# Performance work log

Measured on AMD Instinct MI355X. Metric: run time of the kernel, lower is better.

The kernel has to match this reference:

```python
import jax, jax.numpy as jnp
import numpy as np

B, N, H = 32, 2048, 128


def _lstm_step(c, h, x, Wi, Wh, b):
    # flax LSTMCell: gates i,f,g,o; sigmoid/sigmoid/tanh/sigmoid
    gates = x @ Wi + h @ Wh + b  # (B,N,4H)
    i, f, g, o = jnp.split(gates, 4, axis=-1)
    c_new = jax.nn.sigmoid(f) * c + jax.nn.sigmoid(i) * jnp.tanh(g)
    h_new = jax.nn.sigmoid(o) * jnp.tanh(c_new)
    return c_new, h_new


def setup_inputs() -> dict:
    key = jax.random.key(0)
    ks = jax.random.split(key, 24)
    f32 = jnp.float32
    inp = {}
    inp['node_embeddings'] = jax.random.normal(ks[0], (B, N, H), f32)
    for nm, k in zip(['hs_c0', 'hs_h0', 'hs_c1', 'hs_h1'], ks[1:5]):
        inp[nm] = jax.random.normal(k, (B, N, H), f32)
    ip = jax.random.uniform(ks[5], (B, N), f32)
    inp['instruction_pointer'] = ip / jnp.sum(ip, axis=-1, keepdims=True)
    inp['Wi0'] = jax.random.normal(ks[6], (H, 4 * H), f32) * 0.05
    inp['Wh0'] = jax.random.normal(ks[7], (H, 4 * H), f32) * 0.05
    inp['b0'] = jnp.zeros((4 * H,), f32)
    inp['Wi1'] = jax.random.normal(ks[8], (H, 4 * H), f32) * 0.05
    inp['Wh1'] = jax.random.normal(ks[9], (H, 4 * H), f32) * 0.05
    inp['b1'] = jnp.zeros((4 * H,), f32)
    inp['W_raise'] = jax.random.normal(ks[10], (4 * H, 2), f32) * 0.05
    inp['b_raise'] = jnp.zeros((2,), f32)
    inp['W_branch'] = jax.random.normal(ks[11], (4 * H, 2), f32) * 0.05
    inp['b_branch'] = jnp.zeros((2,), f32)
    inp['true_indexes'] = jax.random.randint(ks[12], (B, N), 0, N, jnp.int32)
    inp['false_indexes'] = jax.random.randint(ks[13], (B, N), 0, N, jnp.int32)
    inp['raise_indexes'] = jax.random.randint(ks[14], (B, N), 0, N, jnp.int32)
    inp['exit_node_indexes'] = jax.random.randint(ks[15], (B,), 0, N, jnp.int32)
    inp['raise_node_indexes'] = jax.random.randint(ks[16], (B,), 0, N, jnp.int32)
    inp['step_limits'] = jax.random.randint(ks[17], (B,), 0, 100, jnp.int32)
    inp['current_step'] = 5
    return inp


def reference(node_embeddings, hs_c0, hs_h0, hs_c1, hs_h1, instruction_pointer,
              Wi0, Wh0, b0, Wi1, Wh1, b1, W_raise, b_raise, W_branch, b_branch,
              true_indexes, false_indexes, raise_indexes,
              exit_node_indexes, raise_node_indexes, step_limits, current_step):
    bidx = jnp.arange(B)
    old = [hs_c0, hs_h0, hs_c1, hs_h1]

    # execute: per-node 2-layer stacked LSTM (vectorized over B,N)
    c0n, h0n = _lstm_step(hs_c0, hs_h0, node_embeddings, Wi0, Wh0, b0)
    c1n, h1n = _lstm_step(hs_c1, hs_h1, h0n, Wi1, Wh1, b1)
    contrib = [c0n, h0n, c1n, h1n]

    # mask_h: keep old state at exit node and (raise_in_ipagnn) at raise node
    def mask_nodes(hc, ho, idx):
        return hc.at[bidx, idx].set(ho[bidx, idx])
    contrib = [mask_nodes(mask_nodes(hc, ho, exit_node_indexes), ho, raise_node_indexes)
               for hc, ho in zip(contrib, old)]

    hs_emb = jnp.concatenate(contrib, axis=-1)  # (B,N,4H)

    raise_dec = jax.nn.softmax(hs_emb @ W_raise + b_raise, axis=-1)
    zero_one = jnp.array([0.0, 1.0], dtype=raise_dec.dtype)
    raise_dec = raise_dec.at[bidx, exit_node_indexes].set(zero_one)
    raise_dec = raise_dec.at[bidx, raise_node_indexes].set(zero_one)
    branch_dec = jax.nn.softmax(hs_emb @ W_branch + b_branch, axis=-1)

    p_raise = raise_dec[..., 0]
    p_noraise = raise_dec[..., 1]
    p_true = p_noraise * branch_dec[..., 0]
    p_false = p_noraise * branch_dec[..., 1]

    seg = jax.vmap(lambda v, idx: jax.ops.segment_sum(v, idx, num_segments=N))
    ip = instruction_pointer
    ip_new = (seg(p_raise * ip, raise_indexes)
              + seg(p_true * ip, true_indexes)
              + seg(p_false * ip, false_indexes))  # (B,N)
    denom = (ip_new + 1e-7)[..., None]

    wr = (p_raise * ip)[..., None]
    wt = (p_true * ip)[..., None]
    wf = (p_false * ip)[..., None]

    def agg(h):
        return (seg(h * wr, raise_indexes) + seg(h * wt, true_indexes)
                + seg(h * wf, false_indexes)) / denom
    hs_new = [agg(h) for h in contrib]

    # keep_old_if_done
    not_done = (current_step < step_limits)  # (B,)
    hs_out = [jnp.where(not_done[:, None, None], hn, ho) for hn, ho in zip(hs_new, old)]
    ip_out = jnp.where(not_done[:, None], ip_new, ip)

    # pack carry: (c0,h0,c1,h1, instruction_pointer) -> (B,N,4H+1)
    return jnp.concatenate(hs_out + [ip_out[..., None]], axis=-1)
```

## Files before the change

### kernel.cpp

```cpp
#include <hip/hip_runtime.h>
#include <stdint.h>

#define BB 32
#define NN 2048
#define HH 128
#define BN (BB*NN)

typedef short v8s __attribute__((ext_vector_type(8)));
typedef float v4f __attribute__((ext_vector_type(4)));

__device__ __forceinline__ unsigned short f2b(float f){
  union { float f; unsigned int i; } v; v.f = f;
  unsigned int x = v.i;
  unsigned int r = x + 0x7FFFu + ((x >> 16) & 1u);
  return (unsigned short)(r >> 16);
}
__device__ __forceinline__ unsigned int pk2(float a, float b){
  return (unsigned int)f2b(a) | ((unsigned int)f2b(b) << 16);
}
__device__ __forceinline__ float b2f(unsigned int s){
  union { unsigned int i; float f; } v; v.i = s << 16; return v.f;
}
__device__ __forceinline__ float frcp(float x){ return __builtin_amdgcn_rcpf(x); }
__device__ __forceinline__ float fsigm(float x){ return frcp(1.0f + __expf(-x)); }
__device__ __forceinline__ float ftanh(float x){ return 1.0f - 2.0f*frcp(1.0f + __expf(2.0f*x)); }

__global__ __launch_bounds__(512) void kswz(
    const float* __restrict__ Wi0, const float* __restrict__ Wh0,
    const float* __restrict__ Wi1, const float* __restrict__ Wh1,
    unsigned short* __restrict__ Bsw0, unsigned short* __restrict__ Bsw1){
  int idx = blockIdx.x*512 + threadIdx.x;
  int bid = idx >> 6;
  int lane = idx & 63;
  int layer = bid >> 8;
  int kc = (bid >> 5) & 7;
  int ct = bid & 31;
  const float* Wi = layer ? Wi1 : Wi0;
  const float* Wh = layer ? Wh1 : Wh0;
  unsigned short* dst = layer ? Bsw1 : Bsw0;
  int col = ct*16 + (lane & 15);
  int kbase = kc*32 + (lane >> 4)*8;
  size_t o = ((size_t)(kc*32 + ct)*64 + (size_t)lane)*8;
  #pragma unroll
  for (int j = 0; j < 8; j++){
    int k = kbase + j;
    dst[o + j] = f2b((k < 128) ? Wi[k*512 + col] : Wh[(k-128)*512 + col]);
  }
}

#define ROWSB 32
#define PA 264
#define PH 136

struct LstmLds {
  unsigned short A[ROWSB*PA];
  unsigned short H[ROWSB*PH];
  unsigned short G[ROWSB*PH];
};
struct CsrLds {
  int cnt[NN];
  int off[NN];
  int cur[NN];
  int wpart[8];
};

__global__ __launch_bounds__(512, 4) void klstm2(
    const float* __restrict__ ne,
    float* __restrict__ c0, float* __restrict__ h0,
    float* __restrict__ c1, float* __restrict__ h1,
    unsigned short* __restrict__ sc0, unsigned short* __restrict__ sh0,
    unsigned short* __restrict__ sc1, unsigned short* __restrict__ sh1,
    const unsigned short* __restrict__ Bsw0, const float* __restrict__ b0,
    const unsigned short* __restrict__ Bsw1, const float* __restrict__ b1,
    const int* __restrict__ exit_idx, const int* __restrict__ raise_idx,
    const int* __restrict__ ri, const int* __restrict__ ti,
    const int* __restrict__ fi,
    int* __restrict__ counts, int* __restrict__ offsets,
    unsigned short* __restrict__ edges,
    const int* __restrict__ step_limits, const int* __restrict__ cur_step,
    int useb)
{
  __shared__ union { LstmLds l; CsrLds c; } u;

  int tid = threadIdx.x;

  if (blockIdx.x < 32){
    int b = blockIdx.x;
    const int* rp = ri + b*NN;
    const int* tp = ti + b*NN;
    const int* fp = fi + b*NN;

    #pragma unroll
    for (int p = 0; p < 4; p++){ u.c.cnt[p*512 + tid] = 0; u.c.cur[p*512 + tid] = 0; }
    __syncthreads();

    int rv[4], tv[4], fv[4];
    #pragma unroll
    for (int p = 0; p < 4; p++){
      int n = p*512 + tid;
      rv[p] = rp[n]; tv[p] = tp[n]; fv[p] = fp[n];
      atomicAdd(&u.c.cnt[rv[p]], 1);
      atomicAdd(&u.c.cnt[tv[p]], 1);
      atomicAdd(&u.c.cnt[fv[p]], 1);
    }
    __syncthreads();

    int cc0 = u.c.cnt[4*tid], cc1 = u.c.cnt[4*tid+1];
    int cc2 = u.c.cnt[4*tid+2], cc3 = u.c.cnt[4*tid+3];
    int s = cc0 + cc1 + cc2 + cc3;
    int lane = tid & 63, wv = tid >> 6;
    int inc = s;
    #pragma unroll
    for (int d = 1; d < 64; d <<= 1){
      int t = __shfl_up(inc, d, 64);
      if (lane >= d) inc += t;
    }
    if (lane == 63) u.c.wpart[wv] = inc;
    __syncthreads();
    if (tid == 0){
      int run = 0;
      #pragma unroll
      for (int w = 0; w < 8; w++){ int t = u.c.wpart[w]; u.c.wpart[w] = run; run += t; }
    }
    __syncthreads();
    int excl = u.c.wpart[wv] + inc - s;
    u.c.off[4*tid]   = excl;
    u.c.off[4*tid+1] = excl + cc0;
    u.c.off[4*tid+2] = excl + cc0 + cc1;
    u.c.off[4*tid+3] = excl + cc0 + cc1 + cc2;
    offsets[b*NN + 4*tid]   = excl;
    offsets[b*NN + 4*tid+1] = excl + cc0;
    offsets[b*NN + 4*tid+2] = excl + cc0 + cc1;
    offsets[b*NN + 4*tid+3] = excl + cc0 + cc1 + cc2;
    counts[b*NN + 4*tid]   = cc0;
    counts[b*NN + 4*tid+1] = cc1;
    counts[b*NN + 4*tid+2] = cc2;
    counts[b*NN + 4*tid+3] = cc3;
    __syncthreads();

    size_t ebase = (size_t)b*3*NN;
    #pragma unroll
    for (int p = 0; p < 4; p++){
      int n = p*512 + tid;
      int t0 = rv[p]; int p0 = atomicAdd(&u.c.cur[t0], 1);
      edges[ebase + u.c.off[t0] + p0] = (unsigned short)n;
      int t1 = tv[p]; int p1 = atomicAdd(&u.c.cur[t1], 1);
      edges[ebase + u.c.off[t1] + p1] = (unsigned short)(n | (1<<11));
      int t2 = fv[p]; int p2 = atomicAdd(&u.c.cur[t2], 1);
      edges[ebase + u.c.off[t2] + p2] = (unsigned short)(n | (2<<11));
    }
    return;
  }

  int rowbase = (blockIdx.x - 32) * ROWSB;
  int b = rowbase >> 11;
  if (cur_step[0] >= step_limits[b]) return;

  int wid = tid >> 6, lane = tid & 63;
  int quad = lane >> 4, l16 = lane & 15;
  int ch = wid*16 + l16;
  int e_row = exit_idx[b], r_row = raise_idx[b];

  #pragma unroll
  for (int p = 0; p < 4; p++){
    int idx = p*512 + tid;
    int row = idx >> 6, chunk = idx & 63;
    size_t g = (size_t)(rowbase + row)*128 + (chunk & 31)*4;
    float4 v = (chunk < 32) ? *(const float4*)(ne + g) : *(const float4*)(h0 + g);
    uint2 w; w.x = pk2(v.x, v.y); w.y = pk2(v.z, v.w);
    *(uint2*)&u.l.A[row*PA + chunk*4] = w;
  }
  __syncthreads();

  float cpre[8], bias[4];
  #pragma unroll
  for (int rt = 0; rt < 2; rt++)
    #pragma unroll
    for (int r = 0; r < 4; r++)
      cpre[rt*4+r] = c0[((size_t)rowbase + rt*16 + quad*4 + r)*128 + ch];
  #pragma unroll
  for (int g = 0; g < 4; g++) bias[g] = b0[g*128 + ch];

  #pragma unroll
  for (int p = 0; p < 2; p++){
    int idx = p*512 + tid;
    int row = idx >> 5, chunk = idx & 31;
    float4 v = *(const float4*)(h1 + (size_t)(rowbase + row)*128 + chunk*4);
    uint2 w; w.x = pk2(v.x, v.y); w.y = pk2(v.z, v.w);
    *(uint2*)&u.l.H[row*PH + chunk*4] = w;
  }

  const v8s* Bv0 = (const v8s*)Bsw0;
  v4f acc[2][4] = {};
  v8s bc[4], bn[4];
  #pragma unroll
  for (int g = 0; g < 4; g++) bc[g] = Bv0[(size_t)(g*8 + wid)*64 + lane];
  #pragma unroll
  for (int kc = 0; kc < 8; kc++){
    if (kc < 7){
      #pragma unroll
      for (int g = 0; g < 4; g++) bn[g] = Bv0[(size_t)((kc+1)*32 + g*8 + wid)*64 + lane];
    }
    v8s a0 = *(const v8s*)&u.l.A[(0*16 + l16)*PA + kc*32 + quad*8];
    v8s a1 = *(const v8s*)&u.l.A[(1*16 + l16)*PA + kc*32 + quad*8];
    #pragma unroll
    for (int g = 0; g < 4; g++){
      acc[0][g] = __builtin_amdgcn_mfma_f32_16x16x32_bf16(a0, bc[g], acc[0][g], 0,0,0);
      acc[1][g] = __builtin_amdgcn_mfma_f32_16x16x32_bf16(a1, bc[g], acc[1][g], 0,0,0);
    }
    #pragma unroll
    for (int g = 0; g < 4; g++) bc[g] = bn[g];
  }

  #pragma unroll
  for (int rt = 0; rt < 2; rt++){
    #pragma unroll
    for (int r = 0; r < 4; r++){
      int k = rt*4 + r;
      int lrow = rt*16 + quad*4 + r;
      int grow = rowbase + lrow;
      int node = grow & 2047;
      bool special = (node == e_row) || (node == r_row);
      float iv = acc[rt][0][r] + bias[0];
      float fv = acc[rt][1][r] + bias[1];
      float gv = acc[rt][2][r] + bias[2];
      float ov = acc[rt][3][r] + bias[3];
      float cn = fsigm(fv)*cpre[k] + fsigm(iv)*ftanh(gv);
      float hn = fsigm(ov)*ftanh(cn);
      if (useb){
        sc0[(size_t)grow*128 + ch] = special ? f2b(cpre[k]) : f2b(cn);
        sh0[(size_t)grow*128 + ch] = special ? u.l.A[lrow*PA + 128 + ch] : f2b(hn);
      } else if (!special){
        c0[(size_t)grow*128 + ch] = cn;
        h0[(size_t)grow*128 + ch] = hn;
      }
      u.l.G[lrow*PH + ch] = f2b(hn);
    }
  }

  #pragma unroll
  for (int rt = 0; rt < 2; rt++)
    #pragma unroll
    for (int r = 0; r < 4; r++)
      cpre[rt*4+r] = c1[((size_t)rowbase + rt*16 + quad*4 + r)*128 + ch];
  #pragma unroll
  for (int g = 0; g < 4; g++) bias[g] = b1[g*128 + ch];
  const v8s* Bv1 = (const v8s*)Bsw1;
  #pragma unroll
  for (int g = 0; g < 4; g++) bc[g] = Bv1[(size_t)(g*8 + wid)*64 + lane];

  __syncthreads();

  #pragma unroll
  for (int rt = 0; rt < 2; rt++)
    #pragma unroll
    for (int g = 0; g < 4; g++)
      acc[rt][g] = (v4f){0.f, 0.f, 0.f, 0.f};
  #pragma unroll
  for (int kc = 0; kc < 8; kc++){
    if (kc < 7){
      #pragma unroll
      for (int g = 0; g < 4; g++) bn[g] = Bv1[(size_t)((kc+1)*32 + g*8 + wid)*64 + lane];
    }
    v8s a0, a1;
    if (kc < 4){
      a0 = *(const v8s*)&u.l.G[(0*16 + l16)*PH + kc*32 + quad*8];
      a1 = *(const v8s*)&u.l.G[(1*16 + l16)*PH + kc*32 + quad*8];
    } else {
      a0 = *(const v8s*)&u.l.H[(0*16 + l16)*PH + (kc-4)*32 + quad*8];
      a1 = *(const v8s*)&u.l.H[(1*16 + l16)*PH + (kc-4)*32 + quad*8];
    }
    #pragma unroll
    for (int g = 0; g < 4; g++){
      acc[0][g] = __builtin_amdgcn_mfma_f32_16x16x32_bf16(a0, bc[g], acc[0][g], 0,0,0);
      acc[1][g] = __builtin_amdgcn_mfma_f32_16x16x32_bf16(a1, bc[g], acc[1][g], 0,0,0);
    }
    #pragma unroll
    for (int g = 0; g < 4; g++) bc[g] = bn[g];
  }

  #pragma unroll
  for (int rt = 0; rt < 2; rt++){
    #pragma unroll
    for (int r = 0; r < 4; r++){
      int k = rt*4 + r;
      int lrow = rt*16 + quad*4 + r;
      int grow = rowbase + lrow;
      int node = grow & 2047;
      bool special = (node == e_row) || (node == r_row);
      float iv = acc[rt][0][r] + bias[0];
      float fv = acc[rt][1][r] + bias[1];
      float gv = acc[rt][2][r] + bias[2];
      float ov = acc[rt][3][r] + bias[3];
      float cn = fsigm(fv)*cpre[k] + fsigm(iv)*ftanh(gv);
      float hn = fsigm(ov)*ftanh(cn);
      if (useb){
        sc1[(size_t)grow*128 + ch] = special ? f2b(cpre[k]) : f2b(cn);
        sh1[(size_t)grow*128 + ch] = special ? u.l.H[lrow*PH + ch] : f2b(hn);
      } else if (!special){
        c1[(size_t)grow*128 + ch] = cn;
        h1[(size_t)grow*128 + ch] = hn;
      }
    }
  }
}

__global__ __launch_bounds__(256) void kdec(
    const float* __restrict__ c0, const float* __restrict__ h0,
    const float* __restrict__ c1, const float* __restrict__ h1,
    const unsigned short* __restrict__ sc0, const unsigned short* __restrict__ sh0,
    const unsigned short* __restrict__ sc1, const unsigned short* __restrict__ sh1,
    const float* __restrict__ Wr, const float* __restrict__ br,
    const float* __restrict__ Wb, const float* __restrict__ bb,
    const float* __restrict__ ip,
    const int* __restrict__ exit_idx, const int* __restrict__ raise_idx,
    float* __restrict__ wbuf, int useb)
{
  int tid = threadIdx.x;
  int wid = tid >> 6, lane = tid & 63;
  int gid = blockIdx.x*4 + wid;
  int b = gid >> 11, n = gid & 2047;

  float hv[8];
  if (useb){
    const unsigned short* bufs16[4] = {sc0, sh0, sc1, sh1};
    const unsigned short* hb = bufs16[lane >> 4] + (size_t)gid*128 + (lane & 15)*8;
    uint4 raw = *(const uint4*)hb;
    hv[0] = b2f(raw.x & 0xffffu); hv[1] = b2f(raw.x >> 16);
    hv[2] = b2f(raw.y & 0xffffu); hv[3] = b2f(raw.y >> 16);
    hv[4] = b2f(raw.z & 0xffffu); hv[5] = b2f(raw.z >> 16);
    hv[6] = b2f(raw.w & 0xffffu); hv[7] = b2f(raw.w >> 16);
  } else {
    const float* bufs[4] = {c0, h0, c1, h1};
    const float* hb = bufs[lane >> 4] + (size_t)gid*128 + (lane & 15)*8;
    float4 hv0 = *(const float4*)hb;
    float4 hv1 = *(const float4*)(hb + 4);
    hv[0]=hv0.x; hv[1]=hv0.y; hv[2]=hv0.z; hv[3]=hv0.w;
    hv[4]=hv1.x; hv[5]=hv1.y; hv[6]=hv1.z; hv[7]=hv1.w;
  }
  const float* wrp = Wr + lane*16;
  const float* wbp = Wb + lane*16;
  float r0=0.f, r1=0.f, q0=0.f, q1=0.f;
  #pragma unroll
  for (int j = 0; j < 8; j++){
    float h = hv[j];
    r0 += h * wrp[j*2];  r1 += h * wrp[j*2+1];
    q0 += h * wbp[j*2];  q1 += h * wbp[j*2+1];
  }
  #pragma unroll
  for (int off = 32; off > 0; off >>= 1){
    r0 += __shfl_xor(r0, off, 64);
    r1 += __shfl_xor(r1, off, 64);
    q0 += __shfl_xor(q0, off, 64);
    q1 += __shfl_xor(q1, off, 64);
  }
  if (lane == 0){
    r0 += br[0]; r1 += br[1];
    q0 += bb[0]; q1 += bb[1];
    float pr, pn;
    if (n == exit_idx[b] || n == raise_idx[b]){ pr = 0.f; pn = 1.f; }
    else {
      float m = fmaxf(r0, r1);
      float e0 = __expf(r0 - m), e1 = __expf(r1 - m);
      pr = e0 / (e0 + e1); pn = e1 / (e0 + e1);
    }
    float m2 = fmaxf(q0, q1);
    float f0 = __expf(q0 - m2), f1 = __expf(q1 - m2);
    float pt = f0 / (f0 + f1), pf = f1 / (f0 + f1);
    float ipv = ip[gid];
    wbuf[0*BN + gid] = pr * ipv;
    wbuf[1*BN + gid] = pn * pt * ipv;
    wbuf[2*BN + gid] = pn * pf * ipv;
  }
}

__global__ __launch_bounds__(512) void kagg(
    const float* __restrict__ c0, const float* __restrict__ h0,
    const float* __restrict__ c1, const float* __restrict__ h1,
    const unsigned short* __restrict__ sc0, const unsigned short* __restrict__ sh0,
    const unsigned short* __restrict__ sc1, const unsigned short* __restrict__ sh1,
    const float* __restrict__ ip,
    const float* __restrict__ wbuf, const unsigned short* __restrict__ edges,
    const int* __restrict__ counts, const int* __restrict__ offsets,
    const int* __restrict__ step_limits, const int* __restrict__ cur_step,
    float* __restrict__ out, int useb)
{
  int tid0 = threadIdx.x;
  int sub = tid0 >> 7;
  int tid = tid0 & 127;
  int gid = blockIdx.x*4 + sub;
  int b = gid >> 11;
  size_t obase = (size_t)gid*513;
  const float* bufs[4] = {c0, h0, c1, h1};

  if (cur_step[0] >= step_limits[b]){
    int c = tid*4;
    const float* s = bufs[c >> 7];
    size_t rb = (size_t)gid*128 + (c & 127);
    __builtin_nontemporal_store(s[rb+0], &out[obase + c+0]);
    __builtin_nontemporal_store(s[rb+1], &out[obase + c+1]);
    __builtin_nontemporal_store(s[rb+2], &out[obase + c+2]);
    __builtin_nontemporal_store(s[rb+3], &out[obase + c+3]);
    if (tid == 0) __builtin_nontemporal_store(ip[gid], &out[obase + 512]);
    return;
  }

  int cnt = counts[gid], off = offsets[gid];
  const unsigned short* eb = edges + (size_t)b*3*NN + off;
  int lane = tid & 63;
  int coff = (tid & 31)*4;
  float a0=0.f, a1=0.f, a2=0.f, a3=0.f, ipn=0.f;

  if (useb){
    const unsigned short* bufs16[4] = {sc0, sh0, sc1, sh1};
    const unsigned short* sb = bufs16[tid >> 5];
    for (int base = 0; base < cnt; base += 64){
      int e = base + lane;
      int n_l = 0; float w_l = 0.f;
      if (e < cnt){
        int pk = eb[e];
        n_l = pk & 2047;
        w_l = wbuf[(pk >> 11)*BN + (b<<11) + n_l];
      }
      int m = min(cnt - base, 64);
      for (int j = 0; j < m; j++){
        int   n = __shfl(n_l, j, 64);
        float w = __shfl(w_l, j, 64);
        uint2 raw = *(const uint2*)(sb + ((size_t)(b<<11) + n)*128 + coff);
        ipn += w;
        a0 += w * b2f(raw.x & 0xffffu);
        a1 += w * b2f(raw.x >> 16);
        a2 += w * b2f(raw.y & 0xffffu);
        a3 += w * b2f(raw.y >> 16);
      }
    }
  } else {
    const float* sb = bufs[tid >> 5];
    for (int base = 0; base < cnt; base += 64){
      int e = base + lane;
      int n_l = 0; float w_l = 0.f;
      if (e < cnt){
        int pk = eb[e];
        n_l = pk & 2047;
        w_l = wbuf[(pk >> 11)*BN + (b<<11) + n_l];
      }
      int m = min(cnt - base, 64);
      for (int j = 0; j < m; j++){
        int   n = __shfl(n_l, j, 64);
        float w = __shfl(w_l, j, 64);
        float4 sv = *(const float4*)(sb + ((size_t)(b<<11) + n)*128 + coff);
        ipn += w;
        a0 += w * sv.x;
        a1 += w * sv.y;
        a2 += w * sv.z;
        a3 += w * sv.w;
      }
    }
  }
  int c = tid*4;
  float inv = 1.0f / (ipn + 1e-7f);
  __builtin_nontemporal_store(a0*inv, &out[obase + c+0]);
  __builtin_nontemporal_store(a1*inv, &out[obase + c+1]);
  __builtin_nontemporal_store(a2*inv, &out[obase + c+2]);
  __builtin_nontemporal_store(a3*inv, &out[obase + c+3]);
  if (tid == 0) __builtin_nontemporal_store(ipn, &out[obase + 512]);
}

extern "C" void kernel_launch(void* const* d_in, const int* in_sizes, int n_in,
                              void* d_out, int out_size, void* d_ws, size_t ws_size,
                              hipStream_t stream){
  const float* ne  = (const float*)d_in[0];
  float* c0  = (float*)d_in[1];
  float* h0  = (float*)d_in[2];
  float* c1  = (float*)d_in[3];
  float* h1  = (float*)d_in[4];
  const float* ip  = (const float*)d_in[5];
  const float* Wi0 = (const float*)d_in[6];
  const float* Wh0 = (const float*)d_in[7];
  const float* b0  = (const float*)d_in[8];
  const float* Wi1 = (const float*)d_in[9];
  const float* Wh1 = (const float*)d_in[10];
  const float* b1  = (const float*)d_in[11];
  const float* Wr  = (const float*)d_in[12];
  const float* br  = (const float*)d_in[13];
  const float* Wb  = (const float*)d_in[14];
  const float* bb  = (const float*)d_in[15];
  const int* ti  = (const int*)d_in[16];
  const int* fi  = (const int*)d_in[17];
  const int* ri  = (const int*)d_in[18];
  const int* ei  = (const int*)d_in[19];
  const int* rni = (const int*)d_in[20];
  const int* sl  = (const int*)d_in[21];
  const int* cs  = (const int*)d_in[22];
  float* out = (float*)d_out;

  uint8_t* ws = (uint8_t*)d_ws;
  unsigned short* Bsw0    = (unsigned short*)(ws + 0);
  unsigned short* Bsw1    = (unsigned short*)(ws + 262144);
  float*          wbuf    = (float*)(ws + 655360);
  int*            counts  = (int*)(ws + 1441792);
  int*            offsets = (int*)(ws + 1703936);
  unsigned short* edges   = (unsigned short*)(ws + 2228224);
  const size_t SBASE = 2621440;
  const size_t SB    = (size_t)BN * 128 * 2;
  int useb = (ws_size >= SBASE + 4*SB) ? 1 : 0;
  unsigned short* sc0 = (unsigned short*)(ws + SBASE + 0*SB);
  unsigned short* sh0 = (unsigned short*)(ws + SBASE + 1*SB);
  unsigned short* sc1 = (unsigned short*)(ws + SBASE + 2*SB);
  unsigned short* sh1 = (unsigned short*)(ws + SBASE + 3*SB);

  kswz<<<64, 512, 0, stream>>>(Wi0, Wh0, Wi1, Wh1, Bsw0, Bsw1);

  klstm2<<<32 + BN/ROWSB, 512, 0, stream>>>(ne, c0, h0, c1, h1,
                                            sc0, sh0, sc1, sh1,
                                            Bsw0, b0, Bsw1, b1,
                                            ei, rni, ri, ti, fi,
                                            counts, offsets, edges,
                                            sl, cs, useb);

  kdec<<<BN/4, 256, 0, stream>>>(c0, h0, c1, h1, sc0, sh0, sc1, sh1,
                                 Wr, br, Wb, bb, ip, ei, rni, wbuf, useb);

  kagg<<<BN/4, 512, 0, stream>>>(c0, h0, c1, h1, sc0, sh0, sc1, sh1,
                                 ip, wbuf, edges, counts, offsets,
                                 sl, cs, out, useb);
}
```

Baseline: 419.2 us.

## Interleave bf16 LSTM states per node and deepen weight prefetch

```diff
diff --git a/kernel.cpp b/kernel.cpp
--- a/kernel.cpp
+++ b/kernel.cpp
@@ -68,8 +68,7 @@
     const float* __restrict__ ne,
     float* __restrict__ c0, float* __restrict__ h0,
     float* __restrict__ c1, float* __restrict__ h1,
-    unsigned short* __restrict__ sc0, unsigned short* __restrict__ sh0,
-    unsigned short* __restrict__ sc1, unsigned short* __restrict__ sh1,
+    unsigned short* __restrict__ sAll,
     const unsigned short* __restrict__ Bsw0, const float* __restrict__ b0,
     const unsigned short* __restrict__ Bsw1, const float* __restrict__ b1,
     const int* __restrict__ exit_idx, const int* __restrict__ raise_idx,
@@ -192,14 +191,16 @@
 
   const v8s* Bv0 = (const v8s*)Bsw0;
   v4f acc[2][4] = {};
-  v8s bc[4], bn[4];
-  #pragma unroll
-  for (int g = 0; g < 4; g++) bc[g] = Bv0[(size_t)(g*8 + wid)*64 + lane];
+  v8s bc[4], bp1[4], bp2[4];
+  #pragma unroll
+  for (int g = 0; g < 4; g++) bc[g]  = Bv0[(size_t)(0*32 + g*8 + wid)*64 + lane];
+  #pragma unroll
+  for (int g = 0; g < 4; g++) bp1[g] = Bv0[(size_t)(1*32 + g*8 + wid)*64 + lane];
   #pragma unroll
   for (int kc = 0; kc < 8; kc++){
-    if (kc < 7){
+    if (kc < 6){
       #pragma unroll
-      for (int g = 0; g < 4; g++) bn[g] = Bv0[(size_t)((kc+1)*32 + g*8 + wid)*64 + lane];
+      for (int g = 0; g < 4; g++) bp2[g] = Bv0[(size_t)((kc+2)*32 + g*8 + wid)*64 + lane];
     }
     v8s a0 = *(const v8s*)&u.l.A[(0*16 + l16)*PA + kc*32 + quad*8];
     v8s a1 = *(const v8s*)&u.l.A[(1*16 + l16)*PA + kc*32 + quad*8];
@@ -209,7 +210,7 @@
       acc[1][g] = __builtin_amdgcn_mfma_f32_16x16x32_bf16(a1, bc[g], acc[1][g], 0,0,0);
     }
     #pragma unroll
-    for (int g = 0; g < 4; g++) bc[g] = bn[g];
+    for (int g = 0; g < 4; g++){ bc[g] = bp1[g]; bp1[g] = bp2[g]; }
   }
 
   #pragma unroll
@@ -228,8 +229,10 @@
       float cn = fsigm(fv)*cpre[k] + fsigm(iv)*ftanh(gv);
       float hn = fsigm(ov)*ftanh(cn);
       if (useb){
-        sc0[(size_t)grow*128 + ch] = special ? f2b(cpre[k]) : f2b(cn);
-        sh0[(size_t)grow*128 + ch] = special ? u.l.A[lrow*PA + 128 + ch] : f2b(hn);
+        unsigned short cnb = special ? f2b(cpre[k]) : f2b(cn);
+        unsigned short hnb = special ? u.l.A[lrow*PA + 128 + ch] : f2b(hn);
+        sAll[(size_t)grow*512 +       ch] = cnb;
+        sAll[(size_t)grow*512 + 128 + ch] = hnb;
       } else if (!special){
         c0[(size_t)grow*128 + ch] = cn;
         h0[(size_t)grow*128 + ch] = hn;
@@ -247,7 +250,9 @@
   for (int g = 0; g < 4; g++) bias[g] = b1[g*128 + ch];
   const v8s* Bv1 = (const v8s*)Bsw1;
   #pragma unroll
-  for (int g = 0; g < 4; g++) bc[g] = Bv1[(size_t)(g*8 + wid)*64 + lane];
+  for (int g = 0; g < 4; g++) bc[g]  = Bv1[(size_t)(0*32 + g*8 + wid)*64 + lane];
+  #pragma unroll
+  for (int g = 0; g < 4; g++) bp1[g] = Bv1[(size_t)(1*32 + g*8 + wid)*64 + lane];
 
   __syncthreads();
 
@@ -258,9 +263,9 @@
       acc[rt][g] = (v4f){0.f, 0.f, 0.f, 0.f};
   #pragma unroll
   for (int kc = 0; kc < 8; kc++){
-    if (kc < 7){
+    if (kc < 6){
       #pragma unroll
-      for (int g = 0; g < 4; g++) bn[g] = Bv1[(size_t)((kc+1)*32 + g*8 + wid)*64 + lane];
+      for (int g = 0; g < 4; g++) bp2[g] = Bv1[(size_t)((kc+2)*32 + g*8 + wid)*64 + lane];
     }
     v8s a0, a1;
     if (kc < 4){
@@ -276,7 +281,7 @@
       acc[1][g] = __builtin_amdgcn_mfma_f32_16x16x32_bf16(a1, bc[g], acc[1][g], 0,0,0);
     }
     #pragma unroll
-    for (int g = 0; g < 4; g++) bc[g] = bn[g];
+    for (int g = 0; g < 4; g++){ bc[g] = bp1[g]; bp1[g] = bp2[g]; }
   }
 
   #pragma unroll
@@ -295,8 +300,10 @@
       float cn = fsigm(fv)*cpre[k] + fsigm(iv)*ftanh(gv);
       float hn = fsigm(ov)*ftanh(cn);
       if (useb){
-        sc1[(size_t)grow*128 + ch] = special ? f2b(cpre[k]) : f2b(cn);
-        sh1[(size_t)grow*128 + ch] = special ? u.l.H[lrow*PH + ch] : f2b(hn);
+        unsigned short cnb = special ? f2b(cpre[k]) : f2b(cn);
+        unsigned short hnb = special ? u.l.H[lrow*PH + ch] : f2b(hn);
+        sAll[(size_t)grow*512 + 256 + ch] = cnb;
+        sAll[(size_t)grow*512 + 384 + ch] = hnb;
       } else if (!special){
         c1[(size_t)grow*128 + ch] = cn;
         h1[(size_t)grow*128 + ch] = hn;
@@ -305,11 +312,10 @@
   }
 }
 
-__global__ __launch_bounds__(256) void kdec(
+__global__ __launch_bounds__(512) void kdec(
     const float* __restrict__ c0, const float* __restrict__ h0,
     const float* __restrict__ c1, const float* __restrict__ h1,
-    const unsigned short* __restrict__ sc0, const unsigned short* __restrict__ sh0,
-    const unsigned short* __restrict__ sc1, const unsigned short* __restrict__ sh1,
+    const unsigned short* __restrict__ sAll,
     const float* __restrict__ Wr, const float* __restrict__ br,
     const float* __restrict__ Wb, const float* __restrict__ bb,
     const float* __restrict__ ip,
@@ -318,14 +324,12 @@
 {
   int tid = threadIdx.x;
   int wid = tid >> 6, lane = tid & 63;
-  int gid = blockIdx.x*4 + wid;
+  int gid = blockIdx.x*8 + wid;
   int b = gid >> 11, n = gid & 2047;
 
   float hv[8];
   if (useb){
-    const unsigned short* bufs16[4] = {sc0, sh0, sc1, sh1};
-    const unsigned short* hb = bufs16[lane >> 4] + (size_t)gid*128 + (lane & 15)*8;
-    uint4 raw = *(const uint4*)hb;
+    uint4 raw = *(const uint4*)(sAll + (size_t)gid*512 + lane*8);
     hv[0] = b2f(raw.x & 0xffffu); hv[1] = b2f(raw.x >> 16);
     hv[2] = b2f(raw.y & 0xffffu); hv[3] = b2f(raw.y >> 16);
     hv[4] = b2f(raw.z & 0xffffu); hv[5] = b2f(raw.z >> 16);
@@ -377,8 +381,7 @@
 __global__ __launch_bounds__(512) void kagg(
     const float* __restrict__ c0, const float* __restrict__ h0,
     const float* __restrict__ c1, const float* __restrict__ h1,
-    const unsigned short* __restrict__ sc0, const unsigned short* __restrict__ sh0,
-    const unsigned short* __restrict__ sc1, const unsigned short* __restrict__ sh1,
+    const unsigned short* __restrict__ sAll,
     const float* __restrict__ ip,
     const float* __restrict__ wbuf, const unsigned short* __restrict__ edges,
     const int* __restrict__ counts, const int* __restrict__ offsets,
@@ -408,12 +411,9 @@
   int cnt = counts[gid], off = offsets[gid];
   const unsigned short* eb = edges + (size_t)b*3*NN + off;
   int lane = tid & 63;
-  int coff = (tid & 31)*4;
   float a0=0.f, a1=0.f, a2=0.f, a3=0.f, ipn=0.f;
 
   if (useb){
-    const unsigned short* bufs16[4] = {sc0, sh0, sc1, sh1};
-    const unsigned short* sb = bufs16[tid >> 5];
     for (int base = 0; base < cnt; base += 64){
       int e = base + lane;
       int n_l = 0; float w_l = 0.f;
@@ -426,7 +426,7 @@
       for (int j = 0; j < m; j++){
         int   n = __shfl(n_l, j, 64);
         float w = __shfl(w_l, j, 64);
-        uint2 raw = *(const uint2*)(sb + ((size_t)(b<<11) + n)*128 + coff);
+        uint2 raw = *(const uint2*)(sAll + ((size_t)(b<<11) + n)*512 + tid*4);
         ipn += w;
         a0 += w * b2f(raw.x & 0xffffu);
         a1 += w * b2f(raw.x >> 16);
@@ -436,6 +436,7 @@
     }
   } else {
     const float* sb = bufs[tid >> 5];
+    int coff = (tid & 31)*4;
     for (int base = 0; base < cnt; base += 64){
       int e = base + lane;
       int n_l = 0; float w_l = 0.f;
@@ -502,26 +503,22 @@
   int*            offsets = (int*)(ws + 1703936);
   unsigned short* edges   = (unsigned short*)(ws + 2228224);
   const size_t SBASE = 2621440;
-  const size_t SB    = (size_t)BN * 128 * 2;
-  int useb = (ws_size >= SBASE + 4*SB) ? 1 : 0;
-  unsigned short* sc0 = (unsigned short*)(ws + SBASE + 0*SB);
-  unsigned short* sh0 = (unsigned short*)(ws + SBASE + 1*SB);
-  unsigned short* sc1 = (unsigned short*)(ws + SBASE + 2*SB);
-  unsigned short* sh1 = (unsigned short*)(ws + SBASE + 3*SB);
+  const size_t SB    = (size_t)BN * 512 * 2;
+  int useb = (ws_size >= SBASE + SB) ? 1 : 0;
+  unsigned short* sAll = (unsigned short*)(ws + SBASE);
 
   kswz<<<64, 512, 0, stream>>>(Wi0, Wh0, Wi1, Wh1, Bsw0, Bsw1);
 
-  klstm2<<<32 + BN/ROWSB, 512, 0, stream>>>(ne, c0, h0, c1, h1,
-                                            sc0, sh0, sc1, sh1,
+  klstm2<<<32 + BN/ROWSB, 512, 0, stream>>>(ne, c0, h0, c1, h1, sAll,
                                             Bsw0, b0, Bsw1, b1,
                                             ei, rni, ri, ti, fi,
                                             counts, offsets, edges,
                                             sl, cs, useb);
 
-  kdec<<<BN/4, 256, 0, stream>>>(c0, h0, c1, h1, sc0, sh0, sc1, sh1,
+  kdec<<<BN/8, 512, 0, stream>>>(c0, h0, c1, h1, sAll,
                                  Wr, br, Wb, bb, ip, ei, rni, wbuf, useb);
 
-  kagg<<<BN/4, 512, 0, stream>>>(c0, h0, c1, h1, sc0, sh0, sc1, sh1,
+  kagg<<<BN/4, 512, 0, stream>>>(c0, h0, c1, h1, sAll,
                                  ip, wbuf, edges, counts, offsets,
                                  sl, cs, out, useb);
 }
```

New measurement: 417.1 us. Within noise of the previous version (-0.5%).
